# Performance work log

Hardware: AMD Instinct MI355X
Metric: run time of the kernel (lower is better)

## Reference

```python
import jax, jax.numpy as jnp
import numpy as np

D = 1024
N_HEAD = 16
EXP = 4
EPS = 1e-6


def setup_inputs() -> dict:
    key = jax.random.key(0)
    ks = jax.random.split(key, 7)
    s = 0.02
    return {
        "x": jax.random.normal(ks[0], (2, 2048, D), dtype=jnp.float32),
        "w_qkv": jax.random.normal(ks[1], (3 * D, D), dtype=jnp.float32) * s,
        "w_o": jax.random.normal(ks[2], (D, D), dtype=jnp.float32) * s,
        "w_up": jax.random.normal(ks[3], (EXP * D, D), dtype=jnp.float32) * s,
        "w_gate": jax.random.normal(ks[4], (EXP * D, D), dtype=jnp.float32) * s,
        "w_down": jax.random.normal(ks[5], (D, EXP * D), dtype=jnp.float32) * s,
        "scale1": jnp.ones((D,), dtype=jnp.float32),
        "scale2": jnp.ones((D,), dtype=jnp.float32),
    }


def rmsnorm(x, scale):
    return x / jnp.sqrt(jnp.mean(x * x, axis=-1, keepdims=True) + EPS) * scale


def attention(x, w_qkv, w_o):
    b, s, d = x.shape
    dh = d // N_HEAD
    qkv = x @ w_qkv.T  # [b,s,3d]
    q, k, v = jnp.split(qkv, 3, axis=-1)
    # [b,h,s,dh]
    q = q.reshape(b, s, N_HEAD, dh).transpose(0, 2, 1, 3)
    k = k.reshape(b, s, N_HEAD, dh).transpose(0, 2, 1, 3)
    v = v.reshape(b, s, N_HEAD, dh).transpose(0, 2, 1, 3)
    scores = jnp.einsum("bhqd,bhkd->bhqk", q, k) / jnp.sqrt(jnp.float32(dh))
    causal = jnp.tril(jnp.ones((s, s), dtype=bool))
    scores = jnp.where(causal, scores, -jnp.inf)
    attn = jax.nn.softmax(scores, axis=-1)
    out = jnp.einsum("bhqk,bhkd->bhqd", attn, v)
    out = out.transpose(0, 2, 1, 3).reshape(b, s, d)
    return out @ w_o.T


def mlp(x, w_up, w_gate, w_down):
    return (x @ w_up.T * jax.nn.silu(x @ w_gate.T)) @ w_down.T


def reference(x, w_qkv, w_o, w_up, w_gate, w_down, scale1, scale2):
    x = x + attention(rmsnorm(x, scale1), w_qkv, w_o)
    return x + mlp(rmsnorm(x, scale2), w_up, w_gate, w_down)
```

## Files before the change

kernel.cpp:

```cpp
#include <hip/hip_runtime.h>


typedef __attribute__((ext_vector_type(8))) short short8;
typedef __attribute__((ext_vector_type(4))) float floatx4;

#define EPI_NONE 0
#define EPI_RES  1
#define EPI_GATE 2
#define EPI_QKV  3

#define QSCALE 0.1803368801f

__device__ __forceinline__ float b2f(unsigned short u) {
  union { unsigned int i; float f; } c; c.i = ((unsigned int)u) << 16; return c.f;
}
__device__ __forceinline__ unsigned short f2b(float f) {
  union { float f; unsigned int u; } c; c.f = f;
  unsigned int r = 0x7fffu + ((c.u >> 16) & 1u);
  return (unsigned short)((c.u + r) >> 16);
}
__device__ __forceinline__ unsigned int f2b2(float a, float b) {
  return (unsigned int)f2b(a) | ((unsigned int)f2b(b) << 16);
}

__device__ __forceinline__ void load_lds16(const void* g, void* l) {
  __builtin_amdgcn_global_load_lds(
      (const __attribute__((address_space(1))) unsigned int*)g,
      (__attribute__((address_space(3))) unsigned int*)l, 16, 0, 0);
}

#define GBAR() __builtin_amdgcn_s_barrier()
#define WLG()  asm volatile("s_waitcnt lgkmcnt(0)" ::: "memory")
#define WVM(N) asm volatile("s_waitcnt vmcnt(" #N ")" ::: "memory")

__global__ __launch_bounds__(256)
void cvt_all_kernel(const float* __restrict__ wq, const float* __restrict__ wo,
                    const float* __restrict__ wu, const float* __restrict__ wg,
                    const float* __restrict__ wd,
                    unsigned short* __restrict__ oq, unsigned short* __restrict__ oo,
                    unsigned short* __restrict__ ou, unsigned short* __restrict__ og,
                    unsigned short* __restrict__ od) {
  int i = blockIdx.x * 256 + threadIdx.x;
  const float* src; unsigned short* dst; int k;
  if (i < 786432)        { src = wq; dst = oq; k = i; }
  else if (i < 1048576)  { src = wo; dst = oo; k = i - 786432; }
  else if (i < 2097152)  { src = wu; dst = ou; k = i - 1048576; }
  else if (i < 3145728)  { src = wg; dst = og; k = i - 2097152; }
  else                   { src = wd; dst = od; k = i - 3145728; }
  float4 v = ((const float4*)src)[k];
  ushort4 o;
  o.x = f2b(v.x); o.y = f2b(v.y); o.z = f2b(v.z); o.w = f2b(v.w);
  ((ushort4*)dst)[k] = o;
}

__global__ __launch_bounds__(256)
void rmsnorm_kernel(const float* __restrict__ x,
                    const float* __restrict__ scale,
                    unsigned short* __restrict__ y) {
  const int row = blockIdx.x;
  const int tid = threadIdx.x;
  const int base = row * 1024 + tid * 4;
  float4 v = *(const float4*)(x + base);
  float ss = v.x*v.x + v.y*v.y + v.z*v.z + v.w*v.w;
#pragma unroll
  for (int d = 32; d > 0; d >>= 1) ss += __shfl_down(ss, d);
  __shared__ float red[4];
  const int wave = tid >> 6, lane = tid & 63;
  if (lane == 0) red[wave] = ss;
  __syncthreads();
  float tot = red[0] + red[1] + red[2] + red[3];
  float rs = rsqrtf(tot * (1.0f/1024.0f) + 1e-6f);
  float4 sv = *(const float4*)(scale + tid * 4);
  ushort4 o;
  o.x = f2b(v.x * rs * sv.x);
  o.y = f2b(v.y * rs * sv.y);
  o.z = f2b(v.z * rs * sv.z);
  o.w = f2b(v.w * rs * sv.w);
  *(ushort4*)(y + base) = o;
}

__global__ __launch_bounds__(256)
void rmsnorm_res2_kernel(const float* __restrict__ x,
                         const float* __restrict__ p0,
                         const float* __restrict__ p1,
                         const float* __restrict__ scale,
                         float* __restrict__ x1,
                         unsigned short* __restrict__ y) {
  const int row = blockIdx.x;
  const int tid = threadIdx.x;
  const int base = row * 1024 + tid * 4;
  float4 a = *(const float4*)(x + base);
  float4 b = *(const float4*)(p0 + base);
  float4 c = *(const float4*)(p1 + base);
  float4 v;
  v.x = a.x + b.x + c.x; v.y = a.y + b.y + c.y;
  v.z = a.z + b.z + c.z; v.w = a.w + b.w + c.w;
  *(float4*)(x1 + base) = v;
  float ss = v.x*v.x + v.y*v.y + v.z*v.z + v.w*v.w;
#pragma unroll
  for (int d = 32; d > 0; d >>= 1) ss += __shfl_down(ss, d);
  __shared__ float red[4];
  const int wave = tid >> 6, lane = tid & 63;
  if (lane == 0) red[wave] = ss;
  __syncthreads();
  float tot = red[0] + red[1] + red[2] + red[3];
  float rs = rsqrtf(tot * (1.0f/1024.0f) + 1e-6f);
  float4 sv = *(const float4*)(scale + tid * 4);
  ushort4 o;
  o.x = f2b(v.x * rs * sv.x);
  o.y = f2b(v.y * rs * sv.y);
  o.z = f2b(v.z * rs * sv.z);
  o.w = f2b(v.w * rs * sv.w);
  *(ushort4*)(y + base) = o;
}

__global__ __launch_bounds__(256)
void reduce_out_kernel(const float* __restrict__ x1,
                       const float* __restrict__ p1,
                       float* outp) {
  int i = blockIdx.x * 256 + threadIdx.x;
  float4 a = ((const float4*)x1)[i];
  float4 b = ((const float4*)p1)[i];
  float4 c = ((float4*)outp)[i];
  float4 v;
  v.x = a.x + b.x + c.x; v.y = a.y + b.y + c.y;
  v.z = a.z + b.z + c.z; v.w = a.w + b.w + c.w;
  ((float4*)outp)[i] = v;
}

template<int EPI, typename OutT, typename ResT>
__global__ __launch_bounds__(256)
void gemm_bt(const unsigned short* __restrict__ A,
             const unsigned short* __restrict__ B,
             OutT* C, const ResT* R, unsigned short* VT,
             int M, int N, int K, int ldc) {
  __shared__ __align__(16) unsigned short As[128 * 32];
  __shared__ __align__(16) unsigned short Bs[128 * 32];
  const int tid = threadIdx.x;
  const int wave = tid >> 6;
  const int lane = tid & 63;
  const int m0 = blockIdx.y * 128;
  const int n0 = blockIdx.x * 128;
  const int wm = (wave & 1) * 64;
  const int wn = (wave >> 1) * 64;
  const int frow = lane & 15;
  const int fk = (lane >> 4) * 8;

  floatx4 acc[4][4];
#pragma unroll
  for (int i = 0; i < 4; ++i)
#pragma unroll
    for (int j = 0; j < 4; ++j) acc[i][j] = (floatx4){0.f, 0.f, 0.f, 0.f};

  const int srow = lane >> 2;
  const int scol = (lane & 3) * 8;
  const unsigned short* Ag  = A + (size_t)(m0 + wave * 16 + srow) * K + scol;
  const unsigned short* Ag2 = A + (size_t)(m0 + (wave + 4) * 16 + srow) * K + scol;
  const unsigned short* Bg  = B + (size_t)(n0 + wave * 16 + srow) * K + scol;
  const unsigned short* Bg2 = B + (size_t)(n0 + (wave + 4) * 16 + srow) * K + scol;

  for (int k0 = 0; k0 < K; k0 += 32) {
    __syncthreads();
    load_lds16(Ag + k0,  &As[wave * 512]);
    load_lds16(Ag2 + k0, &As[(wave + 4) * 512]);
    load_lds16(Bg + k0,  &Bs[wave * 512]);
    load_lds16(Bg2 + k0, &Bs[(wave + 4) * 512]);
    __syncthreads();
    short8 af[4], bf[4];
#pragma unroll
    for (int i = 0; i < 4; ++i) af[i] = *(const short8*)&As[(wm + 16*i + frow)*32 + fk];
#pragma unroll
    for (int j = 0; j < 4; ++j) bf[j] = *(const short8*)&Bs[(wn + 16*j + frow)*32 + fk];
#pragma unroll
    for (int i = 0; i < 4; ++i)
#pragma unroll
      for (int j = 0; j < 4; ++j)
        acc[i][j] = __builtin_amdgcn_mfma_f32_16x16x32_bf16(af[i], bf[j], acc[i][j], 0, 0, 0);
  }

  const int g4 = (lane >> 4) * 4;

  if constexpr (EPI == EPI_QKV) {
    if (n0 >= 2048) {
#pragma unroll
      for (int i = 0; i < 4; ++i) {
        const int row0 = m0 + wm + 16*i + g4;
        const int b = row0 >> 11, s0 = row0 & 2047;
#pragma unroll
        for (int j = 0; j < 4; ++j) {
          const int col = n0 + wn + 16*j + frow;
          const int dg = col - 2048;
          const int rowv = (b << 10) + dg;
          ushort4 ov;
          ov.x = f2b(acc[i][j][0]);
          ov.y = f2b(acc[i][j][1]);
          ov.z = f2b(acc[i][j][2]);
          ov.w = f2b(acc[i][j][3]);
          *(ushort4*)(VT + (size_t)rowv * 2048 + s0) = ov;
        }
      }
      return;
    }
  }

  const float qs = (EPI == EPI_QKV && n0 < 1024) ? QSCALE : 1.0f;
#pragma unroll
  for (int i = 0; i < 4; ++i) {
#pragma unroll
    for (int r = 0; r < 4; ++r) {
      const int row = m0 + wm + 16*i + g4 + r;
#pragma unroll
      for (int j = 0; j < 4; ++j) {
        const int col = n0 + wn + 16*j + frow;
        const size_t idx = (size_t)row * ldc + col;
        float v = acc[i][j][r];
        if constexpr (EPI == EPI_RES) {
          v += (float)R[idx];
        } else if constexpr (EPI == EPI_GATE) {
          float up = b2f((unsigned short)R[idx]);
          v = up * (v / (1.f + __expf(-v)));
        } else if constexpr (EPI == EPI_QKV) {
          v *= qs;
        }
        if constexpr (sizeof(OutT) == 4) C[idx] = v;
        else                             C[idx] = f2b(v);
      }
    }
  }
}

__global__ __launch_bounds__(256)
void gemm_bt_splitk(const unsigned short* __restrict__ A,
                    const unsigned short* __restrict__ B,
                    float* __restrict__ P0, float* __restrict__ P1,
                    int M, int N, int K, int Ks) {
  __shared__ __align__(16) unsigned short As[128 * 32];
  __shared__ __align__(16) unsigned short Bs[128 * 32];
  const int tid = threadIdx.x;
  const int wave = tid >> 6;
  const int lane = tid & 63;
  const int m0 = blockIdx.y * 128;
  const int n0 = blockIdx.x * 128;
  const int z = blockIdx.z;
  float* C = z ? P1 : P0;
  const int kbase = z * Ks;
  const int wm = (wave & 1) * 64;
  const int wn = (wave >> 1) * 64;
  const int frow = lane & 15;
  const int fk = (lane >> 4) * 8;

  floatx4 acc[4][4];
#pragma unroll
  for (int i = 0; i < 4; ++i)
#pragma unroll
    for (int j = 0; j < 4; ++j) acc[i][j] = (floatx4){0.f, 0.f, 0.f, 0.f};

  const int srow = lane >> 2;
  const int scol = (lane & 3) * 8;
  const unsigned short* Ag  = A + (size_t)(m0 + wave * 16 + srow) * K + kbase + scol;
  const unsigned short* Ag2 = A + (size_t)(m0 + (wave + 4) * 16 + srow) * K + kbase + scol;
  const unsigned short* Bg  = B + (size_t)(n0 + wave * 16 + srow) * K + kbase + scol;
  const unsigned short* Bg2 = B + (size_t)(n0 + (wave + 4) * 16 + srow) * K + kbase + scol;

  for (int k0 = 0; k0 < Ks; k0 += 32) {
    __syncthreads();
    load_lds16(Ag + k0,  &As[wave * 512]);
    load_lds16(Ag2 + k0, &As[(wave + 4) * 512]);
    load_lds16(Bg + k0,  &Bs[wave * 512]);
    load_lds16(Bg2 + k0, &Bs[(wave + 4) * 512]);
    __syncthreads();
    short8 af[4], bf[4];
#pragma unroll
    for (int i = 0; i < 4; ++i) af[i] = *(const short8*)&As[(wm + 16*i + frow)*32 + fk];
#pragma unroll
    for (int j = 0; j < 4; ++j) bf[j] = *(const short8*)&Bs[(wn + 16*j + frow)*32 + fk];
#pragma unroll
    for (int i = 0; i < 4; ++i)
#pragma unroll
      for (int j = 0; j < 4; ++j)
        acc[i][j] = __builtin_amdgcn_mfma_f32_16x16x32_bf16(af[i], bf[j], acc[i][j], 0, 0, 0);
  }

  const int g4 = (lane >> 4) * 4;
#pragma unroll
  for (int i = 0; i < 4; ++i)
#pragma unroll
    for (int r = 0; r < 4; ++r) {
      const int row = m0 + wm + 16*i + g4 + r;
#pragma unroll
      for (int j = 0; j < 4; ++j) {
        const int col = n0 + wn + 16*j + frow;
        C[(size_t)row * N + col] = acc[i][j][r];
      }
    }
}


#define A_OFF(q,h) (((q)*2+(h))*8192)
#define B_OFF(q,h) (32768 + ((q)*2+(h))*8192)

#define STAGE(LB, SRC, T) do {                                               \
    const unsigned short* _s = (SRC) + (size_t)r0 * 1024 + (T) * 64 + gs;    \
    load_lds16(_s,             &lds[(LB) + wave * 512]);                     \
    load_lds16(_s + 64 * 1024, &lds[(LB) + 4096 + wave * 512]);              \
  } while (0)

#define LDA4(dst, q, h) do {                                                 \
    const unsigned short* _b = &lds[A_OFF(q,h) + arow];                      \
    _Pragma("unroll")                                                        \
    for (int _i = 0; _i < 4; ++_i) {                                         \
      dst[_i][0] = *(const short8*)(_b + _i * 1024 + g0);                    \
      dst[_i][1] = *(const short8*)(_b + _i * 1024 + g1);                    \
    }                                                                        \
  } while (0)

#define LDB2(dst, q, h) do {                                                 \
    const unsigned short* _b = &lds[B_OFF(q,h) + brow];                      \
    _Pragma("unroll")                                                        \
    for (int _j = 0; _j < 2; ++_j) {                                         \
      dst[_j][0] = *(const short8*)(_b + _j * 1024 + g0);                    \
      dst[_j][1] = *(const short8*)(_b + _j * 1024 + g1);                    \
    }                                                                        \
  } while (0)

#define MMQ(aa, bb, IO, JO) do {                                             \
    _Pragma("unroll")                                                        \
    for (int _i = 0; _i < 4; ++_i)                                           \
      _Pragma("unroll")                                                      \
      for (int _j = 0; _j < 2; ++_j) {                                       \
        acc[(IO)+_i][(JO)+_j] = __builtin_amdgcn_mfma_f32_16x16x32_bf16(     \
            aa[_i][0], bb[_j][0], acc[(IO)+_i][(JO)+_j], 0, 0, 0);           \
        acc[(IO)+_i][(JO)+_j] = __builtin_amdgcn_mfma_f32_16x16x32_bf16(     \
            aa[_i][1], bb[_j][1], acc[(IO)+_i][(JO)+_j], 0, 0, 0);           \
      }                                                                      \
  } while (0)

__global__ __launch_bounds__(512, 2)
void gemm256_upgate(const unsigned short* __restrict__ A,
                    const unsigned short* __restrict__ Bu,
                    const unsigned short* __restrict__ Bg,
                    unsigned short* __restrict__ C) {
  extern __shared__ __align__(16) unsigned short lds[];
  const int tid  = threadIdx.x;
  const int wave = tid >> 6;
  const int lane = tid & 63;
  const int wr   = wave >> 2;
  const int wc   = wave & 3;
  const int frow = lane & 15;
  const int s4   = lane >> 4;

  const int orig = blockIdx.x;
  const int swz  = (orig & 7) * 64 + (orig >> 3);
  const int bx   = swz & 31;
  const int by   = swz >> 5;
  const int m0   = by * 256;
  const int n0   = bx * 128;

  const int f7 = frow & 7;
  const int g0 = ((0 + s4) ^ f7) * 8;
  const int g1 = ((4 + s4) ^ f7) * 8;
  const int arow = (wr * 64 + frow) * 64;
  const int brow = (wc * 32 + frow) * 64;

  const int r0 = wave * 8 + (lane >> 3);
  const int gs = ((lane & 7) ^ (lane >> 3)) * 8;

  const unsigned short* Asrc  = A  + (size_t)m0 * 1024;
  const unsigned short* B0src = Bu + (size_t)(bx * 128) * 1024;
  const unsigned short* B1src = Bg + (size_t)(bx * 128) * 1024;

  floatx4 acc[8][4];
#pragma unroll
  for (int i = 0; i < 8; ++i)
#pragma unroll
    for (int j = 0; j < 4; ++j) acc[i][j] = (floatx4){0.f, 0.f, 0.f, 0.f};

  STAGE(A_OFF(0,0), Asrc, 0);
  STAGE(B_OFF(0,0), B0src, 0);
  STAGE(B_OFF(0,1), B1src, 0);
  STAGE(A_OFF(0,1), Asrc + 128 * 1024, 0);
  WVM(4);
  STAGE(A_OFF(1,0), Asrc, 1);
  STAGE(B_OFF(1,0), B0src, 1);
  STAGE(B_OFF(1,1), B1src, 1);
  WVM(6);
  GBAR();

  short8 af0[4][2], af1[4][2], bf0[2][2], bf1[2][2];

  for (int it = 0; it < 8; ++it) {
    const int t   = it * 2;
    const int tn2 = (t + 2) & 15;
    const int tn3 = (t + 3) & 15;
    LDA4(af0, 0, 0);
    LDB2(bf0, 0, 0);
    STAGE(A_OFF(1,1), Asrc + 128 * 1024, (t + 1) & 15);
    GBAR(); WLG();
    __builtin_amdgcn_s_setprio(1); MMQ(af0, bf0, 0, 0); __builtin_amdgcn_s_setprio(0);
    GBAR();
    LDB2(bf1, 0, 1);
    STAGE(A_OFF(0,0), Asrc, tn2);
    GBAR(); WLG();
    __builtin_amdgcn_s_setprio(1); MMQ(af0, bf1, 0, 2); __builtin_amdgcn_s_setprio(0);
    GBAR();
    LDA4(af1, 0, 1);
    STAGE(B_OFF(0,0), B0src, tn2);
    GBAR(); WLG();
    __builtin_amdgcn_s_setprio(1); MMQ(af1, bf0, 4, 0); __builtin_amdgcn_s_setprio(0);
    GBAR();
    STAGE(B_OFF(0,1), B1src, tn2);
    GBAR();
    __builtin_amdgcn_s_setprio(1); MMQ(af1, bf1, 4, 2); __builtin_amdgcn_s_setprio(0);
    WVM(6);
    GBAR();
    LDA4(af0, 1, 0);
    LDB2(bf0, 1, 0);
    STAGE(A_OFF(0,1), Asrc + 128 * 1024, tn2);
    GBAR(); WLG();
    __builtin_amdgcn_s_setprio(1); MMQ(af0, bf0, 0, 0); __builtin_amdgcn_s_setprio(0);
    GBAR();
    LDB2(bf1, 1, 1);
    STAGE(A_OFF(1,0), Asrc, tn3);
    GBAR(); WLG();
    __builtin_amdgcn_s_setprio(1); MMQ(af0, bf1, 0, 2); __builtin_amdgcn_s_setprio(0);
    GBAR();
    LDA4(af1, 1, 1);
    STAGE(B_OFF(1,0), B0src, tn3);
    GBAR(); WLG();
    __builtin_amdgcn_s_setprio(1); MMQ(af1, bf0, 4, 0); __builtin_amdgcn_s_setprio(0);
    GBAR();
    STAGE(B_OFF(1,1), B1src, tn3);
    GBAR();
    __builtin_amdgcn_s_setprio(1); MMQ(af1, bf1, 4, 2); __builtin_amdgcn_s_setprio(0);
    WVM(6);
    GBAR();
  }
  asm volatile("s_waitcnt vmcnt(0)" ::: "memory");

#pragma unroll
  for (int i = 0; i < 8; ++i) {
    const int row = m0 + (i >> 2) * 128 + wr * 64 + (i & 3) * 16 + s4 * 4;
#pragma unroll
    for (int j = 0; j < 2; ++j) {
      const int col = n0 + wc * 32 + j * 16 + frow;
#pragma unroll
      for (int r = 0; r < 4; ++r) {
        const float g = acc[i][j + 2][r];
        const float v = acc[i][j][r] * (g / (1.f + __expf(-g)));
        C[(size_t)(row + r) * 4096 + col] = f2b(v);
      }
    }
  }
}

__global__ __launch_bounds__(256, 2)
void attn_kernel(const unsigned short* __restrict__ qkv,
                 const unsigned short* __restrict__ vt,
                 unsigned short* __restrict__ out) {
  __shared__ __align__(16) unsigned short Ks[2][2][128 * 32];
  __shared__ __align__(16) unsigned short Vs[2][4][64 * 32];
  const int lin = blockIdx.x;
  const int bh = lin & 31;
  const int q_idx = lin >> 5;
  const int qblk = (q_idx < 8) ? (2 * q_idx) : (31 - 2 * q_idx);
  const int b = bh >> 4, h = bh & 15;
  const int tid = threadIdx.x, w = tid >> 6, lane = tid & 63;
  const int f = lane & 15, g = lane >> 4;
  const int fk = g * 8, g4 = g * 4;
  const int fks = (g ^ ((f >> 1) & 3)) * 8;

  const unsigned short* Qb = qkv + (size_t)(b * 2048) * 2048 + h * 64;
  const unsigned short* Kb = Qb + 1024;
  const unsigned short* Vt = vt + ((size_t)(b * 16 + h) * 64) * 2048;

  const int q0 = qblk * 128 + w * 32;
  short8 qf[2][2];
#pragma unroll
  for (int i = 0; i < 2; ++i)
#pragma unroll
    for (int kq = 0; kq < 2; ++kq)
      qf[i][kq] = *(const short8*)(Qb + (size_t)(q0 + 16*i + f) * 2048 + kq * 32 + fk);

  float m_s[2] = {-1e30f, -1e30f}, l_s[2] = {0.f, 0.f};
  floatx4 o[4][2];
#pragma unroll
  for (int mt = 0; mt < 4; ++mt)
#pragma unroll
    for (int i = 0; i < 2; ++i) o[mt][i] = (floatx4){0.f, 0.f, 0.f, 0.f};

  const int srow = lane >> 2;
  const int scolx = ((lane & 3) ^ ((lane >> 3) & 3)) * 8;

  auto stage = [&](int bb, int kb) {
#pragma unroll
    for (int u = 0; u < 2; ++u) {
      const int seg = w + 4 * u;
#pragma unroll
      for (int kq = 0; kq < 2; ++kq)
        load_lds16(Kb + (size_t)(kb * 128 + seg * 16 + srow) * 2048 + kq * 32 + scolx,
                   &Ks[bb][kq][seg * 512]);
    }
#pragma unroll
    for (int c = 0; c < 4; ++c)
      load_lds16(Vt + (size_t)(w * 16 + srow) * 2048 + kb * 128 + c * 32 + scolx,
                 &Vs[bb][c][w * 512]);
  };

  stage(0, 0);

  for (int kb = 0; kb <= qblk; ++kb) {
    const int cur = kb & 1;
    GBAR();
    if (kb < qblk) {
      stage(cur ^ 1, kb + 1);
      WVM(8);
    } else {
      WVM(0);
    }
    GBAR();
    __builtin_amdgcn_sched_barrier(0);

    const bool diag = (kb == qblk);
    const int jhi0 = diag ? 2 * w : 7;
    const int jhi1 = diag ? 2 * w + 1 : 7;

    floatx4 s[8][2];
#pragma unroll
    for (int j = 0; j < 8; ++j) {
      if (j > jhi1) continue;
      short8 kf0 = *(const short8*)&Ks[cur][0][(16*j + f) * 32 + fks];
      short8 kf1 = *(const short8*)&Ks[cur][1][(16*j + f) * 32 + fks];
      __builtin_amdgcn_s_setprio(1);
#pragma unroll
      for (int i = 0; i < 2; ++i) {
        if (j > (i ? jhi1 : jhi0)) continue;
        s[j][i] = (floatx4){0.f, 0.f, 0.f, 0.f};
        s[j][i] = __builtin_amdgcn_mfma_f32_16x16x32_bf16(kf0, qf[i][0], s[j][i], 0, 0, 0);
        s[j][i] = __builtin_amdgcn_mfma_f32_16x16x32_bf16(kf1, qf[i][1], s[j][i], 0, 0, 0);
      }
      __builtin_amdgcn_s_setprio(0);
    }
    if (diag) {
#pragma unroll
      for (int i = 0; i < 2; ++i) {
        const int qo = 32 * w + 16 * i + f;
        const int jh = i ? jhi1 : jhi0;
#pragma unroll
        for (int j = 0; j < 8; ++j) {
          if (j > jh) continue;
#pragma unroll
          for (int r = 0; r < 4; ++r)
            if (16 * j + g4 + r > qo) s[j][i][r] = -1e30f;
        }
      }
    }
#pragma unroll
    for (int i = 0; i < 2; ++i) {
      const int jh = i ? jhi1 : jhi0;
      float mx = -1e30f;
#pragma unroll
      for (int j = 0; j < 8; ++j) {
        if (j > jh) continue;
#pragma unroll
        for (int r = 0; r < 4; ++r) mx = fmaxf(mx, s[j][i][r]);
      }
      mx = fmaxf(mx, __shfl_xor(mx, 16));
      mx = fmaxf(mx, __shfl_xor(mx, 32));
      const float mnew = fmaxf(m_s[i], mx);
      const float alpha = exp2f(m_s[i] - mnew);
      float rs = 0.f;
#pragma unroll
      for (int j = 0; j < 8; ++j) {
        if (j > jh) continue;
#pragma unroll
        for (int r = 0; r < 4; ++r) {
          float pv = exp2f(s[j][i][r] - mnew);
          s[j][i][r] = pv;
          rs += pv;
        }
      }
      rs += __shfl_xor(rs, 16);
      rs += __shfl_xor(rs, 32);
      l_s[i] = l_s[i] * alpha + rs;
      m_s[i] = mnew;
#pragma unroll
      for (int mt = 0; mt < 4; ++mt) o[mt][i] *= alpha;
    }

    const int chi = diag ? w : 3;
#pragma unroll
    for (int c = 0; c < 4; ++c) {
      if (c > chi) continue;
      short8 pb[2];
#pragma unroll
      for (int i = 0; i < 2; ++i) {
        const int jh = i ? jhi1 : jhi0;
        unsigned int P01 = f2b2(s[2*c][i][0], s[2*c][i][1]);
        unsigned int P23 = f2b2(s[2*c][i][2], s[2*c][i][3]);
        unsigned int Q01 = 0u, Q23 = 0u;
        if (2*c + 1 <= jh) {
          Q01 = f2b2(s[2*c+1][i][0], s[2*c+1][i][1]);
          Q23 = f2b2(s[2*c+1][i][2], s[2*c+1][i][3]);
        }
        asm("v_permlane32_swap_b32 %0, %1" : "+v"(P01), "+v"(Q01));
        asm("v_permlane32_swap_b32 %0, %1" : "+v"(P23), "+v"(Q23));
        asm("v_permlane16_swap_b32 %0, %1" : "+v"(P01), "+v"(Q01));
        asm("v_permlane16_swap_b32 %0, %1" : "+v"(P23), "+v"(Q23));
        union { unsigned int d[4]; short8 v; } pbu;
        pbu.d[0] = P01; pbu.d[1] = P23; pbu.d[2] = Q01; pbu.d[3] = Q23;
        pb[i] = pbu.v;
      }
#pragma unroll
      for (int mt = 0; mt < 4; ++mt) {
        short8 va = *(const short8*)&Vs[cur][c][(16*mt + f) * 32 + fks];
        __builtin_amdgcn_s_setprio(1);
#pragma unroll
        for (int i = 0; i < 2; ++i)
          o[mt][i] = __builtin_amdgcn_mfma_f32_16x16x32_bf16(va, pb[i], o[mt][i], 0, 0, 0);
        __builtin_amdgcn_s_setprio(0);
      }
    }
  }

#pragma unroll
  for (int i = 0; i < 2; ++i) {
    const float inv = 1.0f / l_s[i];
    unsigned short* orow = out + (size_t)(b * 2048 + q0 + 16*i + f) * 1024 + h * 64;
#pragma unroll
    for (int mt = 0; mt < 4; ++mt) {
      ushort4 ov;
      ov.x = f2b(o[mt][i][0] * inv);
      ov.y = f2b(o[mt][i][1] * inv);
      ov.z = f2b(o[mt][i][2] * inv);
      ov.w = f2b(o[mt][i][3] * inv);
      *(ushort4*)(orow + 16 * mt + g4) = ov;
    }
  }
}

extern "C" void kernel_launch(void* const* d_in, const int* in_sizes, int n_in,
                              void* d_out, int out_size, void* d_ws, size_t ws_size,
                              hipStream_t stream) {
  const float* x      = (const float*)d_in[0];
  const float* w_qkv  = (const float*)d_in[1];
  const float* w_o    = (const float*)d_in[2];
  const float* w_up   = (const float*)d_in[3];
  const float* w_gate = (const float*)d_in[4];
  const float* w_down = (const float*)d_in[5];
  const float* scale1 = (const float*)d_in[6];
  const float* scale2 = (const float*)d_in[7];

  char* ws = (char*)d_ws;
  unsigned short* wq_b = (unsigned short*)(ws);
  unsigned short* wo_b = (unsigned short*)(ws +  6291456);
  unsigned short* wu_b = (unsigned short*)(ws +  8388608);
  unsigned short* wg_b = (unsigned short*)(ws + 16777216);
  unsigned short* wd_b = (unsigned short*)(ws + 25165824);
  unsigned short* qkv  = (unsigned short*)(ws + 33554432);
  unsigned short* hup  = (unsigned short*)(ws + 33554432);
  unsigned short* vT   = (unsigned short*)(ws + 50331648);
  unsigned short* attnb= (unsigned short*)(ws + 58720256);
  unsigned short* xn   = (unsigned short*)(ws + 67108864);
  float*          x1   = (float*)         (ws + 75497472);
  float*          outp = (float*)d_out;

  float* wo_p0   = (float*)(ws + 33554432);
  float* wo_p1   = (float*)d_out;
  float* down_p0 = (float*)d_out;
  float* down_p1 = (float*)(ws + 8388608);

  const int M = 4096;
  dim3 blk(256);

  static int lds_opted = 0;
  if (!lds_opted) {
    (void)hipFuncSetAttribute((const void*)gemm256_upgate,
                              hipFuncAttributeMaxDynamicSharedMemorySize, 131072);
    lds_opted = 1;
  }

  cvt_all_kernel<<<16384, blk, 0, stream>>>(w_qkv, w_o, w_up, w_gate, w_down,
                                            wq_b, wo_b, wu_b, wg_b, wd_b);

  rmsnorm_kernel<<<4096, blk, 0, stream>>>(x, scale1, xn);
  gemm_bt<EPI_QKV, unsigned short, unsigned short>
      <<<dim3(24, 32), blk, 0, stream>>>(xn, wq_b, qkv, (const unsigned short*)nullptr, vT,
                                         M, 3072, 1024, 2048);
  attn_kernel<<<dim3(512), blk, 0, stream>>>(qkv, vT, attnb);
  gemm_bt_splitk<<<dim3(8, 32, 2), blk, 0, stream>>>(attnb, wo_b, wo_p0, wo_p1,
                                                     M, 1024, 1024, 512);

  rmsnorm_res2_kernel<<<4096, blk, 0, stream>>>(x, wo_p0, wo_p1, scale2, x1, xn);

  gemm256_upgate<<<dim3(512), dim3(512), 131072, stream>>>(xn, wu_b, wg_b, hup);
  gemm_bt_splitk<<<dim3(8, 32, 2), blk, 0, stream>>>(hup, wd_b, down_p0, down_p1,
                                                     M, 1024, 4096, 2048);
  reduce_out_kernel<<<4096, blk, 0, stream>>>(x1, down_p1, outp);

  (void)in_sizes; (void)n_in; (void)out_size; (void)ws_size;
}
```

Measured before the change: 403.2 us.

## Use 8 waves per attention block with one 16-row query tile each

The attention kernel moves from 4 waves each handling 32 query rows to 8 waves each handling 16 rows. Staging of K/V into shared memory is split across the 8 waves, and query tiles are now scheduled largest-first instead of in paired interleaved order. The aim is more waves per CU to hide latency and less register pressure per wave. In exchange, each wave reads K/V fragments from shared memory for only half as many query rows, so there is more LDS traffic per unit of work.

After: 384.5 us. 4.6% less time.

```diff
diff --git a/kernel.cpp b/kernel.cpp
--- a/kernel.cpp
+++ b/kernel.cpp
@@ -453,7 +453,7 @@
   }
 }
 
-__global__ __launch_bounds__(256, 2)
+__global__ __launch_bounds__(512, 4)
 void attn_kernel(const unsigned short* __restrict__ qkv,
                  const unsigned short* __restrict__ vt,
                  unsigned short* __restrict__ out) {
@@ -461,8 +461,7 @@
   __shared__ __align__(16) unsigned short Vs[2][4][64 * 32];
   const int lin = blockIdx.x;
   const int bh = lin & 31;
-  const int q_idx = lin >> 5;
-  const int qblk = (q_idx < 8) ? (2 * q_idx) : (31 - 2 * q_idx);
+  const int qt = 15 - (lin >> 5);
   const int b = bh >> 4, h = bh & 15;
   const int tid = threadIdx.x, w = tid >> 6, lane = tid & 63;
   const int f = lane & 15, g = lane >> 4;
@@ -473,166 +472,138 @@
   const unsigned short* Kb = Qb + 1024;
   const unsigned short* Vt = vt + ((size_t)(b * 16 + h) * 64) * 2048;
 
-  const int q0 = qblk * 128 + w * 32;
-  short8 qf[2][2];
-#pragma unroll
-  for (int i = 0; i < 2; ++i)
-#pragma unroll
-    for (int kq = 0; kq < 2; ++kq)
-      qf[i][kq] = *(const short8*)(Qb + (size_t)(q0 + 16*i + f) * 2048 + kq * 32 + fk);
-
-  float m_s[2] = {-1e30f, -1e30f}, l_s[2] = {0.f, 0.f};
-  floatx4 o[4][2];
-#pragma unroll
-  for (int mt = 0; mt < 4; ++mt)
-#pragma unroll
-    for (int i = 0; i < 2; ++i) o[mt][i] = (floatx4){0.f, 0.f, 0.f, 0.f};
+  const int q0 = qt * 128 + w * 16;
+  short8 qf[2];
+#pragma unroll
+  for (int kq = 0; kq < 2; ++kq)
+    qf[kq] = *(const short8*)(Qb + (size_t)(q0 + f) * 2048 + kq * 32 + fk);
+
+  float m_s = -1e30f, l_s = 0.f;
+  floatx4 o[4];
+#pragma unroll
+  for (int mt = 0; mt < 4; ++mt) o[mt] = (floatx4){0.f, 0.f, 0.f, 0.f};
 
   const int srow = lane >> 2;
   const int scolx = ((lane & 3) ^ ((lane >> 3) & 3)) * 8;
+  const int vc = w >> 1, vh = w & 1;
 
   auto stage = [&](int bb, int kb) {
 #pragma unroll
-    for (int u = 0; u < 2; ++u) {
-      const int seg = w + 4 * u;
-#pragma unroll
-      for (int kq = 0; kq < 2; ++kq)
-        load_lds16(Kb + (size_t)(kb * 128 + seg * 16 + srow) * 2048 + kq * 32 + scolx,
-                   &Ks[bb][kq][seg * 512]);
-    }
-#pragma unroll
-    for (int c = 0; c < 4; ++c)
-      load_lds16(Vt + (size_t)(w * 16 + srow) * 2048 + kb * 128 + c * 32 + scolx,
-                 &Vs[bb][c][w * 512]);
+    for (int kq = 0; kq < 2; ++kq)
+      load_lds16(Kb + (size_t)(kb * 128 + w * 16 + srow) * 2048 + kq * 32 + scolx,
+                 &Ks[bb][kq][w * 512]);
+#pragma unroll
+    for (int u = 0; u < 2; ++u)
+      load_lds16(Vt + (size_t)(vh * 32 + u * 16 + srow) * 2048 + kb * 128 + vc * 32 + scolx,
+                 &Vs[bb][vc][(vh * 32 + u * 16) * 32]);
   };
 
   stage(0, 0);
 
-  for (int kb = 0; kb <= qblk; ++kb) {
+  for (int kb = 0; kb <= qt; ++kb) {
     const int cur = kb & 1;
     GBAR();
-    if (kb < qblk) {
+    if (kb < qt) {
       stage(cur ^ 1, kb + 1);
-      WVM(8);
+      WVM(4);
     } else {
       WVM(0);
     }
     GBAR();
     __builtin_amdgcn_sched_barrier(0);
 
-    const bool diag = (kb == qblk);
-    const int jhi0 = diag ? 2 * w : 7;
-    const int jhi1 = diag ? 2 * w + 1 : 7;
-
-    floatx4 s[8][2];
+    const bool diag = (kb == qt);
+    const int jhi = diag ? w : 7;
+
+    floatx4 s[8];
 #pragma unroll
     for (int j = 0; j < 8; ++j) {
-      if (j > jhi1) continue;
+      if (j > jhi) continue;
       short8 kf0 = *(const short8*)&Ks[cur][0][(16*j + f) * 32 + fks];
       short8 kf1 = *(const short8*)&Ks[cur][1][(16*j + f) * 32 + fks];
       __builtin_amdgcn_s_setprio(1);
-#pragma unroll
-      for (int i = 0; i < 2; ++i) {
-        if (j > (i ? jhi1 : jhi0)) continue;
-        s[j][i] = (floatx4){0.f, 0.f, 0.f, 0.f};
-        s[j][i] = __builtin_amdgcn_mfma_f32_16x16x32_bf16(kf0, qf[i][0], s[j][i], 0, 0, 0);
-        s[j][i] = __builtin_amdgcn_mfma_f32_16x16x32_bf16(kf1, qf[i][1], s[j][i], 0, 0, 0);
-      }
+      s[j] = (floatx4){0.f, 0.f, 0.f, 0.f};
+      s[j] = __builtin_amdgcn_mfma_f32_16x16x32_bf16(kf0, qf[0], s[j], 0, 0, 0);
+      s[j] = __builtin_amdgcn_mfma_f32_16x16x32_bf16(kf1, qf[1], s[j], 0, 0, 0);
       __builtin_amdgcn_s_setprio(0);
     }
     if (diag) {
 #pragma unroll
-      for (int i = 0; i < 2; ++i) {
-        const int qo = 32 * w + 16 * i + f;
-        const int jh = i ? jhi1 : jhi0;
-#pragma unroll
-        for (int j = 0; j < 8; ++j) {
-          if (j > jh) continue;
-#pragma unroll
-          for (int r = 0; r < 4; ++r)
-            if (16 * j + g4 + r > qo) s[j][i][r] = -1e30f;
-        }
-      }
-    }
-#pragma unroll
-    for (int i = 0; i < 2; ++i) {
-      const int jh = i ? jhi1 : jhi0;
+      for (int j = 0; j < 8; ++j) {
+        if (j != w) continue;
+#pragma unroll
+        for (int r = 0; r < 4; ++r)
+          if (g4 + r > f) s[j][r] = -1e30f;
+      }
+    }
+    {
       float mx = -1e30f;
 #pragma unroll
       for (int j = 0; j < 8; ++j) {
-        if (j > jh) continue;
-#pragma unroll
-        for (int r = 0; r < 4; ++r) mx = fmaxf(mx, s[j][i][r]);
+        if (j > jhi) continue;
+#pragma unroll
+        for (int r = 0; r < 4; ++r) mx = fmaxf(mx, s[j][r]);
       }
       mx = fmaxf(mx, __shfl_xor(mx, 16));
       mx = fmaxf(mx, __shfl_xor(mx, 32));
-      const float mnew = fmaxf(m_s[i], mx);
-      const float alpha = exp2f(m_s[i] - mnew);
+      const float mnew = fmaxf(m_s, mx);
+      const float alpha = exp2f(m_s - mnew);
       float rs = 0.f;
 #pragma unroll
       for (int j = 0; j < 8; ++j) {
-        if (j > jh) continue;
+        if (j > jhi) continue;
 #pragma unroll
         for (int r = 0; r < 4; ++r) {
-          float pv = exp2f(s[j][i][r] - mnew);
-          s[j][i][r] = pv;
+          float pv = exp2f(s[j][r] - mnew);
+          s[j][r] = pv;
           rs += pv;
         }
       }
       rs += __shfl_xor(rs, 16);
       rs += __shfl_xor(rs, 32);
-      l_s[i] = l_s[i] * alpha + rs;
-      m_s[i] = mnew;
-#pragma unroll
-      for (int mt = 0; mt < 4; ++mt) o[mt][i] *= alpha;
-    }
-
-    const int chi = diag ? w : 3;
+      l_s = l_s * alpha + rs;
+      m_s = mnew;
+#pragma unroll
+      for (int mt = 0; mt < 4; ++mt) o[mt] *= alpha;
+    }
+
+    const int chi = diag ? (w >> 1) : 3;
 #pragma unroll
     for (int c = 0; c < 4; ++c) {
       if (c > chi) continue;
-      short8 pb[2];
-#pragma unroll
-      for (int i = 0; i < 2; ++i) {
-        const int jh = i ? jhi1 : jhi0;
-        unsigned int P01 = f2b2(s[2*c][i][0], s[2*c][i][1]);
-        unsigned int P23 = f2b2(s[2*c][i][2], s[2*c][i][3]);
-        unsigned int Q01 = 0u, Q23 = 0u;
-        if (2*c + 1 <= jh) {
-          Q01 = f2b2(s[2*c+1][i][0], s[2*c+1][i][1]);
-          Q23 = f2b2(s[2*c+1][i][2], s[2*c+1][i][3]);
-        }
-        asm("v_permlane32_swap_b32 %0, %1" : "+v"(P01), "+v"(Q01));
-        asm("v_permlane32_swap_b32 %0, %1" : "+v"(P23), "+v"(Q23));
-        asm("v_permlane16_swap_b32 %0, %1" : "+v"(P01), "+v"(Q01));
-        asm("v_permlane16_swap_b32 %0, %1" : "+v"(P23), "+v"(Q23));
-        union { unsigned int d[4]; short8 v; } pbu;
-        pbu.d[0] = P01; pbu.d[1] = P23; pbu.d[2] = Q01; pbu.d[3] = Q23;
-        pb[i] = pbu.v;
-      }
+      unsigned int P01 = f2b2(s[2*c][0], s[2*c][1]);
+      unsigned int P23 = f2b2(s[2*c][2], s[2*c][3]);
+      unsigned int Q01 = 0u, Q23 = 0u;
+      if (2*c + 1 <= jhi) {
+        Q01 = f2b2(s[2*c+1][0], s[2*c+1][1]);
+        Q23 = f2b2(s[2*c+1][2], s[2*c+1][3]);
+      }
+      asm("v_permlane32_swap_b32 %0, %1" : "+v"(P01), "+v"(Q01));
+      asm("v_permlane32_swap_b32 %0, %1" : "+v"(P23), "+v"(Q23));
+      asm("v_permlane16_swap_b32 %0, %1" : "+v"(P01), "+v"(Q01));
+      asm("v_permlane16_swap_b32 %0, %1" : "+v"(P23), "+v"(Q23));
+      union { unsigned int d[4]; short8 v; } pbu;
+      pbu.d[0] = P01; pbu.d[1] = P23; pbu.d[2] = Q01; pbu.d[3] = Q23;
 #pragma unroll
       for (int mt = 0; mt < 4; ++mt) {
         short8 va = *(const short8*)&Vs[cur][c][(16*mt + f) * 32 + fks];
         __builtin_amdgcn_s_setprio(1);
-#pragma unroll
-        for (int i = 0; i < 2; ++i)
-          o[mt][i] = __builtin_amdgcn_mfma_f32_16x16x32_bf16(va, pb[i], o[mt][i], 0, 0, 0);
+        o[mt] = __builtin_amdgcn_mfma_f32_16x16x32_bf16(va, pbu.v, o[mt], 0, 0, 0);
         __builtin_amdgcn_s_setprio(0);
       }
     }
   }
 
-#pragma unroll
-  for (int i = 0; i < 2; ++i) {
-    const float inv = 1.0f / l_s[i];
-    unsigned short* orow = out + (size_t)(b * 2048 + q0 + 16*i + f) * 1024 + h * 64;
+  {
+    const float inv = 1.0f / l_s;
+    unsigned short* orow = out + (size_t)(b * 2048 + q0 + f) * 1024 + h * 64;
 #pragma unroll
     for (int mt = 0; mt < 4; ++mt) {
       ushort4 ov;
-      ov.x = f2b(o[mt][i][0] * inv);
-      ov.y = f2b(o[mt][i][1] * inv);
-      ov.z = f2b(o[mt][i][2] * inv);
-      ov.w = f2b(o[mt][i][3] * inv);
+      ov.x = f2b(o[mt][0] * inv);
+      ov.y = f2b(o[mt][1] * inv);
+      ov.z = f2b(o[mt][2] * inv);
+      ov.w = f2b(o[mt][3] * inv);
       *(ushort4*)(orow + 16 * mt + g4) = ov;
     }
   }
@@ -686,7 +657,7 @@
   gemm_bt<EPI_QKV, unsigned short, unsigned short>
       <<<dim3(24, 32), blk, 0, stream>>>(xn, wq_b, qkv, (const unsigned short*)nullptr, vT,
                                          M, 3072, 1024, 2048);
-  attn_kernel<<<dim3(512), blk, 0, stream>>>(qkv, vT, attnb);
+  attn_kernel<<<dim3(512), dim3(512), 0, stream>>>(qkv, vT, attnb);
   gemm_bt_splitk<<<dim3(8, 32, 2), blk, 0, stream>>>(attnb, wo_b, wo_p0, wo_p1,
                                                      M, 1024, 1024, 512);
 
```
